# Kernel optimization log

Measured on AMD Instinct MI355X. Metric: run time of the kernel, lower is better.

Reference implementation:

```python
import jax, jax.numpy as jnp
import numpy as np

N_NODES = 50000
N_EDGES = 800000
F_IN = 64
F_OUT = 64


def setup_inputs() -> dict:
    key = jax.random.key(0)
    k1, k2, k3, k4, k5 = jax.random.split(key, 5)
    x = jax.random.normal(k1, (N_NODES, F_IN), dtype=jnp.float32)
    edge_index = jax.random.randint(k2, (2, N_EDGES), 0, N_NODES, dtype=jnp.int32)
    # PyG GraphConv params: lin_rel (with bias) applied to aggregated neighbors,
    # lin_root (no bias) applied to the node's own features.
    scale = 1.0 / np.sqrt(F_IN)
    W_rel = jax.random.uniform(k3, (F_OUT, F_IN), dtype=jnp.float32, minval=-scale, maxval=scale)
    b_rel = jax.random.uniform(k4, (F_OUT,), dtype=jnp.float32, minval=-scale, maxval=scale)
    W_root = jax.random.uniform(k5, (F_OUT, F_IN), dtype=jnp.float32, minval=-scale, maxval=scale)
    return {"x": x, "W_rel": W_rel, "b_rel": b_rel, "W_root": W_root, "edge_index": edge_index}


def reference(x, W_rel, b_rel, W_root, edge_index):
    # GraphConv (aggr='add'): out = lin_rel(sum_{j in N(i)} x_j) + lin_root(x_i), then ReLU
    src, dst = edge_index[0], edge_index[1]
    # gather neighbor features along edges, scatter-add into destination nodes
    agg = jax.ops.segment_sum(x[src], dst, num_segments=x.shape[0])  # [N, F_IN]
    out = agg @ W_rel.T + b_rel + x @ W_root.T  # [N, F_OUT]
    return jax.nn.relu(out)
```

## Files before the change

kernel.cpp:

```cpp
#include <hip/hip_runtime.h>

#define F 64
#define TILE 64
#define CAP 2048
#define PAD 65
#define CNTP 16
#define NT_MAX 1024
#define BIN_BLOCKS 128


__global__ __launch_bounds__(256) void bin_kernel(
    const int* __restrict__ edge_index, int* __restrict__ tileCnt,
    unsigned* __restrict__ tileBuf, int n_edges, int n_tiles) {
  __shared__ int hist[NT_MAX];
  __shared__ int gbase[NT_MAX];

  const int t = threadIdx.x;
  for (int i = t; i < n_tiles; i += 256) hist[i] = 0;
  __syncthreads();

  const int per = (n_edges + gridDim.x - 1) / gridDim.x;
  const int e0 = blockIdx.x * per;
  const int e1 = min(e0 + per, n_edges);

  for (int e = e0 + t; e < e1; e += 256)
    atomicAdd(&hist[edge_index[n_edges + e] >> 6], 1);
  __syncthreads();

  for (int i = t; i < n_tiles; i += 256) {
    const int c = hist[i];
    gbase[i] = (c > 0) ? atomicAdd(&tileCnt[i * CNTP], c) : 0;
    hist[i] = 0;
  }
  __syncthreads();

  for (int e = e0 + t; e < e1; e += 256) {
    const int src = edge_index[e];
    const int dst = edge_index[n_edges + e];
    const int tile = dst >> 6;
    const int pos = gbase[tile] + atomicAdd(&hist[tile], 1);
    if (pos < CAP)
      tileBuf[(size_t)tile * CAP + pos] =
          ((unsigned)dst << 16) | (unsigned)src;
  }
}

__global__ __launch_bounds__(256) void transpose_w_kernel(
    const float* __restrict__ W_rel, const float* __restrict__ W_root,
    float* __restrict__ WTrel, float* __restrict__ WTroot) {
  int t = blockIdx.x * 256 + threadIdx.x;
  if (t < F * F) {
    int o = t >> 6, k = t & 63;
    WTrel[k * F + o] = W_rel[t];
    WTroot[k * F + o] = W_root[t];
  }
}

__global__ __launch_bounds__(256) void tile_sort_gather_gemm_kernel(
    const float* __restrict__ x,
    const float* __restrict__ WTrel,
    const float* __restrict__ b_rel,
    const float* __restrict__ WTroot,
    const int* __restrict__ tileCnt,
    const unsigned* __restrict__ tileBuf,
    float* __restrict__ out, int n_nodes) {
  __shared__ float aggT[F * PAD];
  __shared__ float xT[F * PAD];
  __shared__ unsigned short ssrc[CAP + 64];
  __shared__ int hist[TILE];
  __shared__ int soff[TILE + 1];
  __shared__ int scur[TILE];

  const int t = threadIdx.x;
  const int lane = t & 63;
  const int w = t >> 6;
  const int tile = blockIdx.x;
  const int node0 = tile * TILE;
  const int cnt = min(tileCnt[tile * CNTP], CAP);
  const unsigned* lst = tileBuf + (size_t)tile * CAP;

  if (t < TILE) hist[t] = 0;
  if (t < 64) ssrc[cnt + t] = 0;
  {
    const int c4 = t & 15;
    const int rr = t >> 4;
#pragma unroll
    for (int p = 0; p < 4; ++p) {
      const int r = p * 16 + rr;
      const int gi = node0 + r;
      float4 v = make_float4(0.f, 0.f, 0.f, 0.f);
      if (gi < n_nodes) v = *(const float4*)(x + (size_t)gi * F + c4 * 4);
      xT[(c4 * 4 + 0) * PAD + r] = v.x;
      xT[(c4 * 4 + 1) * PAD + r] = v.y;
      xT[(c4 * 4 + 2) * PAD + r] = v.z;
      xT[(c4 * 4 + 3) * PAD + r] = v.w;
    }
  }
  __syncthreads();

  for (int i = t; i < cnt; i += 256) atomicAdd(&hist[(lst[i] >> 16) & 63], 1);
  __syncthreads();

  if (w == 0) {
    int v = hist[lane];
    int incl = v;
#pragma unroll
    for (int d = 1; d < 64; d <<= 1) {
      int up = __shfl_up(incl, d, 64);
      if (lane >= d) incl += up;
    }
    soff[lane] = incl - v;
    scur[lane] = incl - v;
    if (lane == 63) soff[64] = incl;
  }
  __syncthreads();

  for (int i = t; i < cnt; i += 256) {
    const unsigned e = lst[i];
    const int d = (int)((e >> 16) & 63);
    const int pos = atomicAdd(&scur[d], 1);
    ssrc[pos] = (unsigned short)(e & 0xFFFFu);
  }
  __syncthreads();

  const int slot = lane >> 4;
  const int fq = lane & 15;
  for (int nn = 0; nn < 16; ++nn) {
    const int d = w * 16 + nn;
    const int start = soff[d];
    const int end = soff[d + 1];
    float4 acc = make_float4(0.f, 0.f, 0.f, 0.f);
    for (int e0 = start; e0 < end; e0 += 64) {
      const int m = min(64, end - e0);
      for (int b = 0; b < m; b += 16) {
        const int i0 = b + slot, i1 = b + 4 + slot, i2 = b + 8 + slot,
                  i3 = b + 12 + slot;
        const int s0 = (int)ssrc[e0 + i0];
        const int s1 = (int)ssrc[e0 + i1];
        const int s2 = (int)ssrc[e0 + i2];
        const int s3 = (int)ssrc[e0 + i3];
        const float4 f0 = *(const float4*)(x + (size_t)s0 * F + fq * 4);
        const float4 f1 = *(const float4*)(x + (size_t)s1 * F + fq * 4);
        const float4 f2 = *(const float4*)(x + (size_t)s2 * F + fq * 4);
        const float4 f3 = *(const float4*)(x + (size_t)s3 * F + fq * 4);
        acc.x += (i0 < m ? f0.x : 0.f); acc.y += (i0 < m ? f0.y : 0.f);
        acc.z += (i0 < m ? f0.z : 0.f); acc.w += (i0 < m ? f0.w : 0.f);
        acc.x += (i1 < m ? f1.x : 0.f); acc.y += (i1 < m ? f1.y : 0.f);
        acc.z += (i1 < m ? f1.z : 0.f); acc.w += (i1 < m ? f1.w : 0.f);
        acc.x += (i2 < m ? f2.x : 0.f); acc.y += (i2 < m ? f2.y : 0.f);
        acc.z += (i2 < m ? f2.z : 0.f); acc.w += (i2 < m ? f2.w : 0.f);
        acc.x += (i3 < m ? f3.x : 0.f); acc.y += (i3 < m ? f3.y : 0.f);
        acc.z += (i3 < m ? f3.z : 0.f); acc.w += (i3 < m ? f3.w : 0.f);
      }
    }
    acc.x += __shfl_xor(acc.x, 16, 64); acc.y += __shfl_xor(acc.y, 16, 64);
    acc.z += __shfl_xor(acc.z, 16, 64); acc.w += __shfl_xor(acc.w, 16, 64);
    acc.x += __shfl_xor(acc.x, 32, 64); acc.y += __shfl_xor(acc.y, 32, 64);
    acc.z += __shfl_xor(acc.z, 32, 64); acc.w += __shfl_xor(acc.w, 32, 64);
    if (slot == 0) {
      aggT[(fq * 4 + 0) * PAD + d] = acc.x;
      aggT[(fq * 4 + 1) * PAD + d] = acc.y;
      aggT[(fq * 4 + 2) * PAD + d] = acc.z;
      aggT[(fq * 4 + 3) * PAD + d] = acc.w;
    }
  }
  __syncthreads();

  const int oq = t & 15, rq = t >> 4;
  const int o0 = oq * 4, r0 = rq * 4;
  const float4 bias = *(const float4*)(b_rel + o0);
  float acc[4][4];
#pragma unroll
  for (int ri = 0; ri < 4; ++ri) {
    acc[ri][0] = bias.x; acc[ri][1] = bias.y;
    acc[ri][2] = bias.z; acc[ri][3] = bias.w;
  }
#pragma unroll 4
  for (int k = 0; k < F; ++k) {
    const float4 wr = *(const float4*)(WTrel + k * F + o0);
    const float4 wo = *(const float4*)(WTroot + k * F + o0);
    const float a0 = aggT[k * PAD + r0 + 0], a1 = aggT[k * PAD + r0 + 1];
    const float a2 = aggT[k * PAD + r0 + 2], a3 = aggT[k * PAD + r0 + 3];
    const float x0 = xT[k * PAD + r0 + 0], x1 = xT[k * PAD + r0 + 1];
    const float x2 = xT[k * PAD + r0 + 2], x3 = xT[k * PAD + r0 + 3];
    acc[0][0] += a0 * wr.x + x0 * wo.x; acc[0][1] += a0 * wr.y + x0 * wo.y;
    acc[0][2] += a0 * wr.z + x0 * wo.z; acc[0][3] += a0 * wr.w + x0 * wo.w;
    acc[1][0] += a1 * wr.x + x1 * wo.x; acc[1][1] += a1 * wr.y + x1 * wo.y;
    acc[1][2] += a1 * wr.z + x1 * wo.z; acc[1][3] += a1 * wr.w + x1 * wo.w;
    acc[2][0] += a2 * wr.x + x2 * wo.x; acc[2][1] += a2 * wr.y + x2 * wo.y;
    acc[2][2] += a2 * wr.z + x2 * wo.z; acc[2][3] += a2 * wr.w + x2 * wo.w;
    acc[3][0] += a3 * wr.x + x3 * wo.x; acc[3][1] += a3 * wr.y + x3 * wo.y;
    acc[3][2] += a3 * wr.z + x3 * wo.z; acc[3][3] += a3 * wr.w + x3 * wo.w;
  }
#pragma unroll
  for (int ri = 0; ri < 4; ++ri) {
    const int gi = node0 + r0 + ri;
    if (gi < n_nodes) {
      float4 o4;
      o4.x = fmaxf(acc[ri][0], 0.f); o4.y = fmaxf(acc[ri][1], 0.f);
      o4.z = fmaxf(acc[ri][2], 0.f); o4.w = fmaxf(acc[ri][3], 0.f);
      *(float4*)(out + (size_t)gi * F + o0) = o4;
    }
  }
}

extern "C" void kernel_launch(void* const* d_in, const int* in_sizes, int n_in,
                              void* d_out, int out_size, void* d_ws, size_t ws_size,
                              hipStream_t stream) {
  const float* x      = (const float*)d_in[0];
  const float* W_rel  = (const float*)d_in[1];
  const float* b_rel  = (const float*)d_in[2];
  const float* W_root = (const float*)d_in[3];
  const int* edge_index = (const int*)d_in[4];

  const int n_nodes = in_sizes[0] / F;
  const int n_edges = in_sizes[4] / 2;
  const int n_tiles = (n_nodes + TILE - 1) / TILE;

  int* tileCnt      = (int*)d_ws;
  unsigned* tileBuf = (unsigned*)(tileCnt + (size_t)n_tiles * CNTP);
  float* WTrel      = (float*)(tileBuf + (size_t)n_tiles * CAP);
  float* WTroot     = WTrel + F * F;

  float* out = (float*)d_out;

  hipMemsetAsync(tileCnt, 0, (size_t)n_tiles * CNTP * sizeof(int), stream);

  transpose_w_kernel<<<(F * F + 255) / 256, 256, 0, stream>>>(W_rel, W_root,
                                                              WTrel, WTroot);

  bin_kernel<<<BIN_BLOCKS, 256, 0, stream>>>(edge_index, tileCnt, tileBuf,
                                             n_edges, n_tiles);

  tile_sort_gather_gemm_kernel<<<n_tiles, 256, 0, stream>>>(
      x, WTrel, b_rel, WTroot, tileCnt, tileBuf, out, n_nodes);
}
```

Baseline: 148.2 us.

## Merge memset into prep kernel, drop xT staging, shrink shared memory for occupancy

Folds the tileCnt memset and weight transpose into one prep kernel to save a launch. The main kernel no longer stages x into transposed shared memory; it reads self rows directly from global and stores the aggregate row-major with float4 accesses, which roughly halves shared memory and adds a launch_bounds occupancy hint. The gather loop now steps 16 edges at a time with clamped indices, and the bin kernel uses twice as many blocks. The trade-off is extra global reads of x in the GEMM phase and possible register pressure under the occupancy bound.

```diff
diff --git a/kernel.cpp b/kernel.cpp
--- a/kernel.cpp
+++ b/kernel.cpp
@@ -3,11 +3,25 @@
 #define F 64
 #define TILE 64
 #define CAP 2048
-#define PAD 65
+#define PADC 68
 #define CNTP 16
 #define NT_MAX 1024
-#define BIN_BLOCKS 128
-
+#define BIN_BLOCKS 256
+
+
+
+__global__ __launch_bounds__(256) void prep_kernel(
+    const float* __restrict__ W_rel, const float* __restrict__ W_root,
+    float* __restrict__ WTrel, float* __restrict__ WTroot,
+    int* __restrict__ tileCnt, int n_cnt) {
+  const int idx = blockIdx.x * 256 + threadIdx.x;
+  if (idx < F * F) {
+    const int o = idx >> 6, k = idx & 63;
+    WTrel[k * F + o] = W_rel[idx];
+    WTroot[k * F + o] = W_root[idx];
+  }
+  for (int i = idx; i < n_cnt; i += gridDim.x * 256) tileCnt[i] = 0;
+}
 
 __global__ __launch_bounds__(256) void bin_kernel(
     const int* __restrict__ edge_index, int* __restrict__ tileCnt,
@@ -45,18 +59,7 @@
   }
 }
 
-__global__ __launch_bounds__(256) void transpose_w_kernel(
-    const float* __restrict__ W_rel, const float* __restrict__ W_root,
-    float* __restrict__ WTrel, float* __restrict__ WTroot) {
-  int t = blockIdx.x * 256 + threadIdx.x;
-  if (t < F * F) {
-    int o = t >> 6, k = t & 63;
-    WTrel[k * F + o] = W_rel[t];
-    WTroot[k * F + o] = W_root[t];
-  }
-}
-
-__global__ __launch_bounds__(256) void tile_sort_gather_gemm_kernel(
+__global__ __launch_bounds__(256, 6) void tile_sort_gather_gemm_kernel(
     const float* __restrict__ x,
     const float* __restrict__ WTrel,
     const float* __restrict__ b_rel,
@@ -64,8 +67,7 @@
     const int* __restrict__ tileCnt,
     const unsigned* __restrict__ tileBuf,
     float* __restrict__ out, int n_nodes) {
-  __shared__ float aggT[F * PAD];
-  __shared__ float xT[F * PAD];
+  __shared__ float agg[TILE * PADC];
   __shared__ unsigned short ssrc[CAP + 64];
   __shared__ int hist[TILE];
   __shared__ int soff[TILE + 1];
@@ -80,22 +82,7 @@
   const unsigned* lst = tileBuf + (size_t)tile * CAP;
 
   if (t < TILE) hist[t] = 0;
-  if (t < 64) ssrc[cnt + t] = 0;
-  {
-    const int c4 = t & 15;
-    const int rr = t >> 4;
-#pragma unroll
-    for (int p = 0; p < 4; ++p) {
-      const int r = p * 16 + rr;
-      const int gi = node0 + r;
-      float4 v = make_float4(0.f, 0.f, 0.f, 0.f);
-      if (gi < n_nodes) v = *(const float4*)(x + (size_t)gi * F + c4 * 4);
-      xT[(c4 * 4 + 0) * PAD + r] = v.x;
-      xT[(c4 * 4 + 1) * PAD + r] = v.y;
-      xT[(c4 * 4 + 2) * PAD + r] = v.z;
-      xT[(c4 * 4 + 3) * PAD + r] = v.w;
-    }
-  }
+  if (t < 64 && cnt + t < CAP + 64) ssrc[cnt + t] = 0;
   __syncthreads();
 
   for (int i = t; i < cnt; i += 256) atomicAdd(&hist[(lst[i] >> 16) & 63], 1);
@@ -125,49 +112,50 @@
 
   const int slot = lane >> 4;
   const int fq = lane & 15;
+#pragma unroll 2
   for (int nn = 0; nn < 16; ++nn) {
     const int d = w * 16 + nn;
     const int start = soff[d];
     const int end = soff[d + 1];
     float4 acc = make_float4(0.f, 0.f, 0.f, 0.f);
-    for (int e0 = start; e0 < end; e0 += 64) {
-      const int m = min(64, end - e0);
-      for (int b = 0; b < m; b += 16) {
-        const int i0 = b + slot, i1 = b + 4 + slot, i2 = b + 8 + slot,
-                  i3 = b + 12 + slot;
-        const int s0 = (int)ssrc[e0 + i0];
-        const int s1 = (int)ssrc[e0 + i1];
-        const int s2 = (int)ssrc[e0 + i2];
-        const int s3 = (int)ssrc[e0 + i3];
-        const float4 f0 = *(const float4*)(x + (size_t)s0 * F + fq * 4);
-        const float4 f1 = *(const float4*)(x + (size_t)s1 * F + fq * 4);
-        const float4 f2 = *(const float4*)(x + (size_t)s2 * F + fq * 4);
-        const float4 f3 = *(const float4*)(x + (size_t)s3 * F + fq * 4);
-        acc.x += (i0 < m ? f0.x : 0.f); acc.y += (i0 < m ? f0.y : 0.f);
-        acc.z += (i0 < m ? f0.z : 0.f); acc.w += (i0 < m ? f0.w : 0.f);
-        acc.x += (i1 < m ? f1.x : 0.f); acc.y += (i1 < m ? f1.y : 0.f);
-        acc.z += (i1 < m ? f1.z : 0.f); acc.w += (i1 < m ? f1.w : 0.f);
-        acc.x += (i2 < m ? f2.x : 0.f); acc.y += (i2 < m ? f2.y : 0.f);
-        acc.z += (i2 < m ? f2.z : 0.f); acc.w += (i2 < m ? f2.w : 0.f);
-        acc.x += (i3 < m ? f3.x : 0.f); acc.y += (i3 < m ? f3.y : 0.f);
-        acc.z += (i3 < m ? f3.z : 0.f); acc.w += (i3 < m ? f3.w : 0.f);
-      }
+    const int i0 = slot, i1 = 4 + slot, i2 = 8 + slot, i3 = 12 + slot;
+    for (int e0 = start; e0 < end; e0 += 16) {
+      const int m = end - e0;
+      const int j0 = (i0 < m) ? e0 + i0 : cnt;
+      const int j1 = (i1 < m) ? e0 + i1 : cnt;
+      const int j2 = (i2 < m) ? e0 + i2 : cnt;
+      const int j3 = (i3 < m) ? e0 + i3 : cnt;
+      const int s0 = (int)ssrc[j0];
+      const int s1 = (int)ssrc[j1];
+      const int s2 = (int)ssrc[j2];
+      const int s3 = (int)ssrc[j3];
+      const float4 f0 = *(const float4*)(x + (size_t)s0 * F + fq * 4);
+      const float4 f1 = *(const float4*)(x + (size_t)s1 * F + fq * 4);
+      const float4 f2 = *(const float4*)(x + (size_t)s2 * F + fq * 4);
+      const float4 f3 = *(const float4*)(x + (size_t)s3 * F + fq * 4);
+      acc.x += (i0 < m ? f0.x : 0.f); acc.y += (i0 < m ? f0.y : 0.f);
+      acc.z += (i0 < m ? f0.z : 0.f); acc.w += (i0 < m ? f0.w : 0.f);
+      acc.x += (i1 < m ? f1.x : 0.f); acc.y += (i1 < m ? f1.y : 0.f);
+      acc.z += (i1 < m ? f1.z : 0.f); acc.w += (i1 < m ? f1.w : 0.f);
+      acc.x += (i2 < m ? f2.x : 0.f); acc.y += (i2 < m ? f2.y : 0.f);
+      acc.z += (i2 < m ? f2.z : 0.f); acc.w += (i2 < m ? f2.w : 0.f);
+      acc.x += (i3 < m ? f3.x : 0.f); acc.y += (i3 < m ? f3.y : 0.f);
+      acc.z += (i3 < m ? f3.z : 0.f); acc.w += (i3 < m ? f3.w : 0.f);
     }
     acc.x += __shfl_xor(acc.x, 16, 64); acc.y += __shfl_xor(acc.y, 16, 64);
     acc.z += __shfl_xor(acc.z, 16, 64); acc.w += __shfl_xor(acc.w, 16, 64);
     acc.x += __shfl_xor(acc.x, 32, 64); acc.y += __shfl_xor(acc.y, 32, 64);
     acc.z += __shfl_xor(acc.z, 32, 64); acc.w += __shfl_xor(acc.w, 32, 64);
-    if (slot == 0) {
-      aggT[(fq * 4 + 0) * PAD + d] = acc.x;
-      aggT[(fq * 4 + 1) * PAD + d] = acc.y;
-      aggT[(fq * 4 + 2) * PAD + d] = acc.z;
-      aggT[(fq * 4 + 3) * PAD + d] = acc.w;
-    }
+    if (slot == 0) *(float4*)&agg[d * PADC + fq * 4] = acc;
   }
   __syncthreads();
 
   const int oq = t & 15, rq = t >> 4;
   const int o0 = oq * 4, r0 = rq * 4;
+  const float* xp0 = x + (size_t)min(node0 + r0 + 0, n_nodes - 1) * F;
+  const float* xp1 = x + (size_t)min(node0 + r0 + 1, n_nodes - 1) * F;
+  const float* xp2 = x + (size_t)min(node0 + r0 + 2, n_nodes - 1) * F;
+  const float* xp3 = x + (size_t)min(node0 + r0 + 3, n_nodes - 1) * F;
   const float4 bias = *(const float4*)(b_rel + o0);
   float acc[4][4];
 #pragma unroll
@@ -176,21 +164,32 @@
     acc[ri][2] = bias.z; acc[ri][3] = bias.w;
   }
 #pragma unroll 4
-  for (int k = 0; k < F; ++k) {
-    const float4 wr = *(const float4*)(WTrel + k * F + o0);
-    const float4 wo = *(const float4*)(WTroot + k * F + o0);
-    const float a0 = aggT[k * PAD + r0 + 0], a1 = aggT[k * PAD + r0 + 1];
-    const float a2 = aggT[k * PAD + r0 + 2], a3 = aggT[k * PAD + r0 + 3];
-    const float x0 = xT[k * PAD + r0 + 0], x1 = xT[k * PAD + r0 + 1];
-    const float x2 = xT[k * PAD + r0 + 2], x3 = xT[k * PAD + r0 + 3];
-    acc[0][0] += a0 * wr.x + x0 * wo.x; acc[0][1] += a0 * wr.y + x0 * wo.y;
-    acc[0][2] += a0 * wr.z + x0 * wo.z; acc[0][3] += a0 * wr.w + x0 * wo.w;
-    acc[1][0] += a1 * wr.x + x1 * wo.x; acc[1][1] += a1 * wr.y + x1 * wo.y;
-    acc[1][2] += a1 * wr.z + x1 * wo.z; acc[1][3] += a1 * wr.w + x1 * wo.w;
-    acc[2][0] += a2 * wr.x + x2 * wo.x; acc[2][1] += a2 * wr.y + x2 * wo.y;
-    acc[2][2] += a2 * wr.z + x2 * wo.z; acc[2][3] += a2 * wr.w + x2 * wo.w;
-    acc[3][0] += a3 * wr.x + x3 * wo.x; acc[3][1] += a3 * wr.y + x3 * wo.y;
-    acc[3][2] += a3 * wr.z + x3 * wo.z; acc[3][3] += a3 * wr.w + x3 * wo.w;
+  for (int k0 = 0; k0 < F; k0 += 4) {
+    const float4 a0 = *(const float4*)&agg[(r0 + 0) * PADC + k0];
+    const float4 a1 = *(const float4*)&agg[(r0 + 1) * PADC + k0];
+    const float4 a2 = *(const float4*)&agg[(r0 + 2) * PADC + k0];
+    const float4 a3 = *(const float4*)&agg[(r0 + 3) * PADC + k0];
+    const float4 q0 = *(const float4*)(xp0 + k0);
+    const float4 q1 = *(const float4*)(xp1 + k0);
+    const float4 q2 = *(const float4*)(xp2 + k0);
+    const float4 q3 = *(const float4*)(xp3 + k0);
+#pragma unroll
+    for (int kk = 0; kk < 4; ++kk) {
+      const float4 wr = *(const float4*)(WTrel + (k0 + kk) * F + o0);
+      const float4 wo = *(const float4*)(WTroot + (k0 + kk) * F + o0);
+      const float aa0 = ((const float*)&a0)[kk], xx0 = ((const float*)&q0)[kk];
+      const float aa1 = ((const float*)&a1)[kk], xx1 = ((const float*)&q1)[kk];
+      const float aa2 = ((const float*)&a2)[kk], xx2 = ((const float*)&q2)[kk];
+      const float aa3 = ((const float*)&a3)[kk], xx3 = ((const float*)&q3)[kk];
+      acc[0][0] += aa0 * wr.x + xx0 * wo.x; acc[0][1] += aa0 * wr.y + xx0 * wo.y;
+      acc[0][2] += aa0 * wr.z + xx0 * wo.z; acc[0][3] += aa0 * wr.w + xx0 * wo.w;
+      acc[1][0] += aa1 * wr.x + xx1 * wo.x; acc[1][1] += aa1 * wr.y + xx1 * wo.y;
+      acc[1][2] += aa1 * wr.z + xx1 * wo.z; acc[1][3] += aa1 * wr.w + xx1 * wo.w;
+      acc[2][0] += aa2 * wr.x + xx2 * wo.x; acc[2][1] += aa2 * wr.y + xx2 * wo.y;
+      acc[2][2] += aa2 * wr.z + xx2 * wo.z; acc[2][3] += aa2 * wr.w + xx2 * wo.w;
+      acc[3][0] += aa3 * wr.x + xx3 * wo.x; acc[3][1] += aa3 * wr.y + xx3 * wo.y;
+      acc[3][2] += aa3 * wr.z + xx3 * wo.z; acc[3][3] += aa3 * wr.w + xx3 * wo.w;
+    }
   }
 #pragma unroll
   for (int ri = 0; ri < 4; ++ri) {
@@ -224,10 +223,10 @@
 
   float* out = (float*)d_out;
 
-  hipMemsetAsync(tileCnt, 0, (size_t)n_tiles * CNTP * sizeof(int), stream);
-
-  transpose_w_kernel<<<(F * F + 255) / 256, 256, 0, stream>>>(W_rel, W_root,
-                                                              WTrel, WTroot);
+  const int n_cnt = n_tiles * CNTP;
+  const int gPrep = (n_cnt + 255) / 256;
+  prep_kernel<<<gPrep, 256, 0, stream>>>(W_rel, W_root, WTrel, WTroot,
+                                         tileCnt, n_cnt);
 
   bin_kernel<<<BIN_BLOCKS, 256, 0, stream>>>(edge_index, tileCnt, tileBuf,
                                              n_edges, n_tiles);
```

Measured after the change: 273.8 us. +84.8%, slower.
